# Performance work log

Measured on AMD Instinct MI355X. Metric: run time of the kernel, lower is better.

## Reference

```python
import jax, jax.numpy as jnp
import numpy as np

N = 8192
IN_F = 512
OUT_F = 256
ALPHA = 0.2          # LeakyReLU negative slope
MASK_VAL = -9e15     # same sentinel as the torch code


def setup_inputs() -> dict:
    key = jax.random.key(0)
    k1, k2, k3, k4, k5, k6 = jax.random.split(key, 6)
    inputs = jax.random.normal(k1, (N, IN_F), dtype=jnp.float32)
    # sparse-ish 0/1 dense adjacency (~avg degree 64)
    adj = (jax.random.uniform(k2, (N, N)) < (64.0 / N)).astype(jnp.float32)
    W = jax.random.normal(k3, (IN_F, OUT_F), dtype=jnp.float32) * (1.414 / np.sqrt(IN_F))
    a = jax.random.normal(k4, (2 * OUT_F, 1), dtype=jnp.float32) * 0.1
    W_gc = jax.random.normal(k5, (IN_F, OUT_F), dtype=jnp.float32) * (1.414 / np.sqrt(IN_F))
    b_gc = jax.random.normal(k6, (OUT_F,), dtype=jnp.float32) * 0.01
    return {"inputs": inputs, "adj": adj, "W": W, "a": a, "W_gc": W_gc, "b_gc": b_gc}


def reference(inputs, adj, W, a, W_gc, b_gc):
    # h: [n, F]
    h = inputs @ W
    F = h.shape[1]
    # Fused additive attention: e[i,j] = leaky_relu(a1.h_i + a2.h_j)
    # (mathematically identical to the repeat/cat construction in the source)
    f_src = h @ a[:F, 0]   # [n]
    f_dst = h @ a[F:, 0]   # [n]
    e = jax.nn.leaky_relu(f_src[:, None] + f_dst[None, :], negative_slope=ALPHA)  # [n, n]
    # masked row-softmax over neighbors
    att = jnp.where(adj > 0, e, MASK_VAL)
    att = jax.nn.softmax(att, axis=1)
    # dropout p=0.0 -> identity
    h_prime = att @ h  # [n, F]
    # optional dense graph-convolution branch (graph_convolve=True)
    gc = adj @ (inputs @ W_gc) + b_gc
    return h_prime + gc
```

## Files before the change

kernel.cpp:

```cpp
#include <hip/hip_runtime.h>
#include <hip/hip_bf16.h>
#include <math.h>

#define N_NODES 8192
#define IN_F    512
#define OUT_F   256
#define NCAT    512
#define ALPHA   0.2f
#define MAXDEG  512

typedef __attribute__((ext_vector_type(8))) short short8;
typedef __attribute__((ext_vector_type(4))) float f32x4;

static __device__ __forceinline__ short f2bf(float f) {
    union { float f; unsigned u; } v; v.f = f;
    unsigned r = v.u + 0x7fffu + ((v.u >> 16) & 1u);
    return (short)(r >> 16);
}
static __device__ __forceinline__ float bf2f(short s) {
    union { unsigned u; float f; } v;
    v.u = ((unsigned)(unsigned short)s) << 16;
    return v.f;
}

__global__ __launch_bounds__(512) void bt_pack(const float* __restrict__ W,
                                               const float* __restrict__ W_gc,
                                               short* __restrict__ Bt) {
    const int n = blockIdx.x;
    const int k = threadIdx.x;
    const int c = n >> 1;
    float v = (n & 1) ? W_gc[(size_t)k * OUT_F + c] : W[(size_t)k * OUT_F + c];
    Bt[(size_t)n * IN_F + k] = f2bf(v);
}

__global__ __launch_bounds__(256) void gemm_mfma(const float* __restrict__ A,
                                                 const short* __restrict__ Bt,
                                                 short* __restrict__ hcat) {
    __shared__ short As[128 * 32];
    __shared__ short Bs[128 * 32];

    const int tid  = threadIdx.x;
    const int m0   = blockIdx.y * 128;
    const int n0   = blockIdx.x * 128;
    const int wid  = tid >> 6;
    const int lane = tid & 63;
    const int wr   = wid >> 1;
    const int wc   = wid & 1;
    const int mh   = lane & 15;
    const int q    = lane >> 4;

    const int srow  = tid >> 1;
    const int shalf = tid & 1;

    const f32x4 vzero = {0.f, 0.f, 0.f, 0.f};
    f32x4 acc[4][4];
    #pragma unroll
    for (int i = 0; i < 4; i++)
        #pragma unroll
        for (int j = 0; j < 4; j++) acc[i][j] = vzero;

    const float* aga = A  + (size_t)(m0 + srow) * IN_F + shalf * 16;
    const short* bgb = Bt + (size_t)(n0 + srow) * IN_F + shalf * 16;
    short* asw = &As[srow * 32 + shalf * 16];
    short* bsw = &Bs[srow * 32 + shalf * 16];

    for (int k0 = 0; k0 < IN_F; k0 += 32) {
        const float4* a4 = (const float4*)(aga + k0);
        float4 x0 = a4[0], x1 = a4[1], x2 = a4[2], x3 = a4[3];
        const int4* b4 = (const int4*)(bgb + k0);
        int4 bv0 = b4[0], bv1 = b4[1];

        short8 p0, p1;
        p0[0] = f2bf(x0.x); p0[1] = f2bf(x0.y); p0[2] = f2bf(x0.z); p0[3] = f2bf(x0.w);
        p0[4] = f2bf(x1.x); p0[5] = f2bf(x1.y); p0[6] = f2bf(x1.z); p0[7] = f2bf(x1.w);
        p1[0] = f2bf(x2.x); p1[1] = f2bf(x2.y); p1[2] = f2bf(x2.z); p1[3] = f2bf(x2.w);
        p1[4] = f2bf(x3.x); p1[5] = f2bf(x3.y); p1[6] = f2bf(x3.z); p1[7] = f2bf(x3.w);

        __syncthreads();
        *(short8*)asw       = p0;
        *(short8*)(asw + 8) = p1;
        *(int4*)bsw         = bv0;
        *(int4*)(bsw + 8)   = bv1;
        __syncthreads();

        short8 af[4], bfm[4];
        #pragma unroll
        for (int i = 0; i < 4; i++) {
            af[i]  = *(const short8*)&As[(wr * 64 + i * 16 + mh) * 32 + q * 8];
            bfm[i] = *(const short8*)&Bs[(wc * 64 + i * 16 + mh) * 32 + q * 8];
        }
        #pragma unroll
        for (int mi = 0; mi < 4; mi++)
            #pragma unroll
            for (int ni = 0; ni < 4; ni++)
                acc[mi][ni] = __builtin_amdgcn_mfma_f32_16x16x32_bf16(
                    af[mi], bfm[ni], acc[mi][ni], 0, 0, 0);
    }

    #pragma unroll
    for (int mi = 0; mi < 4; mi++)
        #pragma unroll
        for (int ni = 0; ni < 4; ni++) {
            const int col   = n0 + wc * 64 + ni * 16 + mh;
            const int rbase = m0 + wr * 64 + mi * 16 + q * 4;
            f32x4 v = acc[mi][ni];
            #pragma unroll
            for (int r = 0; r < 4; r++)
                hcat[(size_t)(rbase + r) * NCAT + col] = f2bf(v[r]);
        }
}

__global__ __launch_bounds__(256) void compute_f(const short* __restrict__ hcat,
                                                 const float* __restrict__ a,
                                                 float* __restrict__ f_src,
                                                 float* __restrict__ f_dst) {
    const int row  = blockIdx.x * 4 + (threadIdx.x >> 6);
    const int lane = threadIdx.x & 63;
    const short* hr = hcat + (size_t)row * NCAT;
    float s1 = 0.f, s2 = 0.f;
    #pragma unroll
    for (int c = lane; c < OUT_F; c += 64) {
        float hv = bf2f(hr[2 * c]);
        s1 += hv * a[c];
        s2 += hv * a[OUT_F + c];
    }
    #pragma unroll
    for (int off = 32; off; off >>= 1) {
        s1 += __shfl_down(s1, off);
        s2 += __shfl_down(s2, off);
    }
    if (lane == 0) { f_src[row] = s1; f_dst[row] = s2; }
}

__global__ __launch_bounds__(256) void attn_row(const float* __restrict__ adj,
                                                const short* __restrict__ hcat,
                                                const float* __restrict__ f_src,
                                                const float* __restrict__ f_dst,
                                                const float* __restrict__ b_gc,
                                                float* __restrict__ out) {
    __shared__ int   s_idx[MAXDEG];
    __shared__ float s_w[MAXDEG];
    __shared__ float s_red[8];
    __shared__ int   s_count;

    const int row  = blockIdx.x;
    const int tid  = threadIdx.x;
    const int lane = tid & 63;
    const int wid  = tid >> 6;

    if (tid == 0) s_count = 0;
    __syncthreads();

    const float fs = f_src[row];

    const f32x4* arow4 = (const f32x4*)(adj + (size_t)row * N_NODES);
    float lmax = -INFINITY;
    #pragma unroll
    for (int it = 0; it < N_NODES / 4 / 256; it++) {
        const int c = it * 256 + tid;
        f32x4 v = __builtin_nontemporal_load(arow4 + c);
        int cnt = (v[0] > 0.f) + (v[1] > 0.f) + (v[2] > 0.f) + (v[3] > 0.f);
        if (cnt) {
            int pos = atomicAdd(&s_count, cnt);
            const int j0 = c * 4;
            #pragma unroll
            for (int i = 0; i < 4; i++) {
                if (v[i] > 0.f) {
                    float e = fs + f_dst[j0 + i];
                    e = (e > 0.f) ? e : ALPHA * e;
                    s_idx[pos] = j0 + i;
                    s_w[pos]   = e;
                    pos++;
                    lmax = fmaxf(lmax, e);
                }
            }
        }
    }
    #pragma unroll
    for (int off = 32; off; off >>= 1) lmax = fmaxf(lmax, __shfl_down(lmax, off));
    if (lane == 0) s_red[wid] = lmax;
    __syncthreads();
    const float m   = fmaxf(fmaxf(s_red[0], s_red[1]), fmaxf(s_red[2], s_red[3]));
    const int   deg = min(s_count, MAXDEG);

    float lsum = 0.f;
    for (int k = tid; k < deg; k += 256) {
        float w = __expf(s_w[k] - m);
        s_w[k] = w;
        lsum += w;
    }
    #pragma unroll
    for (int off = 32; off; off >>= 1) lsum += __shfl_down(lsum, off);
    if (lane == 0) s_red[4 + wid] = lsum;
    __syncthreads();
    const float l = s_red[4] + s_red[5] + s_red[6] + s_red[7];
    const float inv_l = (deg > 0) ? 1.f / l : 0.f;

    const int u = lane >> 4;
    const int p = lane & 15;
    const short* hbase = hcat + wid * 128 + p * 8;

    float aa0 = 0.f, aa1 = 0.f, aa2 = 0.f, aa3 = 0.f;
    float gg0 = 0.f, gg1 = 0.f, gg2 = 0.f, gg3 = 0.f;
    #pragma unroll 4
    for (int k = u; k < deg; k += 4) {
        const int   j = s_idx[k];
        const float w = s_w[k];
        short8 v = *(const short8*)(hbase + (size_t)j * NCAT);
        aa0 += w * bf2f(v[0]); gg0 += bf2f(v[1]);
        aa1 += w * bf2f(v[2]); gg1 += bf2f(v[3]);
        aa2 += w * bf2f(v[4]); gg2 += bf2f(v[5]);
        aa3 += w * bf2f(v[6]); gg3 += bf2f(v[7]);
    }
    aa0 += __shfl_down(aa0, 32); aa1 += __shfl_down(aa1, 32);
    aa2 += __shfl_down(aa2, 32); aa3 += __shfl_down(aa3, 32);
    gg0 += __shfl_down(gg0, 32); gg1 += __shfl_down(gg1, 32);
    gg2 += __shfl_down(gg2, 32); gg3 += __shfl_down(gg3, 32);
    aa0 += __shfl_down(aa0, 16); aa1 += __shfl_down(aa1, 16);
    aa2 += __shfl_down(aa2, 16); aa3 += __shfl_down(aa3, 16);
    gg0 += __shfl_down(gg0, 16); gg1 += __shfl_down(gg1, 16);
    gg2 += __shfl_down(gg2, 16); gg3 += __shfl_down(gg3, 16);

    if (u == 0) {
        const int col = wid * 64 + p * 4;
        const float4 bg = *(const float4*)(b_gc + col);
        float4 o;
        o.x = aa0 * inv_l + gg0 + bg.x;
        o.y = aa1 * inv_l + gg1 + bg.y;
        o.z = aa2 * inv_l + gg2 + bg.z;
        o.w = aa3 * inv_l + gg3 + bg.w;
        *(float4*)(out + (size_t)row * OUT_F + col) = o;
    }
}

extern "C" void kernel_launch(void* const* d_in, const int* in_sizes, int n_in,
                              void* d_out, int out_size, void* d_ws, size_t ws_size,
                              hipStream_t stream) {
    const float* inputs = (const float*)d_in[0];
    const float* adj    = (const float*)d_in[1];
    const float* W      = (const float*)d_in[2];
    const float* a      = (const float*)d_in[3];
    const float* W_gc   = (const float*)d_in[4];
    const float* b_gc   = (const float*)d_in[5];
    float* out = (float*)d_out;

    short* Bt    = (short*)d_ws;
    short* hcat  = Bt + (size_t)NCAT * IN_F;
    float* f_src = (float*)(hcat + (size_t)N_NODES * NCAT);
    float* f_dst = f_src + N_NODES;

    bt_pack<<<dim3(NCAT), dim3(IN_F), 0, stream>>>(W, W_gc, Bt);
    gemm_mfma<<<dim3(NCAT / 128, N_NODES / 128), 256, 0, stream>>>(inputs, Bt, hcat);
    compute_f<<<N_NODES / 4, 256, 0, stream>>>(hcat, a, f_src, f_dst);
    attn_row<<<N_NODES, 256, 0, stream>>>(adj, hcat, f_src, f_dst, b_gc, out);
}
```

Measured before the change: 432.5 us.

## Split attention into scan and gather kernels with separate h/g tables

Stores the attention features and graph-conv features in two separate bf16 tables instead of one interleaved buffer. The per-row attention kernel is split into a scan pass, which compacts neighbors and exponentiates scores into a global list, and a gather pass, which aggregates h and g rows separately. The softmax max-subtraction is dropped, which saves a reduction and a barrier but risks overflow for large logits. The split adds a kernel launch and a global round-trip for the neighbor list in exchange for lighter, higher-occupancy kernels.

```diff
diff --git a/kernel.cpp b/kernel.cpp
--- a/kernel.cpp
+++ b/kernel.cpp
@@ -10,6 +10,7 @@
 #define MAXDEG  512
 
 typedef __attribute__((ext_vector_type(8))) short short8;
+typedef __attribute__((ext_vector_type(4))) short short4e;
 typedef __attribute__((ext_vector_type(4))) float f32x4;
 
 static __device__ __forceinline__ short f2bf(float f) {
@@ -28,14 +29,15 @@
                                                short* __restrict__ Bt) {
     const int n = blockIdx.x;
     const int k = threadIdx.x;
-    const int c = n >> 1;
-    float v = (n & 1) ? W_gc[(size_t)k * OUT_F + c] : W[(size_t)k * OUT_F + c];
+    float v = (n < OUT_F) ? W[(size_t)k * OUT_F + n]
+                          : W_gc[(size_t)k * OUT_F + (n - OUT_F)];
     Bt[(size_t)n * IN_F + k] = f2bf(v);
 }
 
 __global__ __launch_bounds__(256) void gemm_mfma(const float* __restrict__ A,
                                                  const short* __restrict__ Bt,
-                                                 short* __restrict__ hcat) {
+                                                 short* __restrict__ h_t,
+                                                 short* __restrict__ g_t) {
     __shared__ short As[128 * 32];
     __shared__ short Bs[128 * 32];
 
@@ -97,32 +99,35 @@
                     af[mi], bfm[ni], acc[mi][ni], 0, 0, 0);
     }
 
+    short* tab  = (n0 < OUT_F) ? h_t : g_t;
+    const int cb = (n0 < OUT_F) ? n0 : n0 - OUT_F;
     #pragma unroll
     for (int mi = 0; mi < 4; mi++)
         #pragma unroll
         for (int ni = 0; ni < 4; ni++) {
-            const int col   = n0 + wc * 64 + ni * 16 + mh;
+            const int col   = cb + wc * 64 + ni * 16 + mh;
             const int rbase = m0 + wr * 64 + mi * 16 + q * 4;
             f32x4 v = acc[mi][ni];
             #pragma unroll
             for (int r = 0; r < 4; r++)
-                hcat[(size_t)(rbase + r) * NCAT + col] = f2bf(v[r]);
+                tab[(size_t)(rbase + r) * OUT_F + col] = f2bf(v[r]);
         }
 }
 
-__global__ __launch_bounds__(256) void compute_f(const short* __restrict__ hcat,
+__global__ __launch_bounds__(256) void compute_f(const short* __restrict__ h_t,
                                                  const float* __restrict__ a,
                                                  float* __restrict__ f_src,
                                                  float* __restrict__ f_dst) {
     const int row  = blockIdx.x * 4 + (threadIdx.x >> 6);
     const int lane = threadIdx.x & 63;
-    const short* hr = hcat + (size_t)row * NCAT;
+    const int c0   = lane * 4;
+    short4e v = *(const short4e*)(h_t + (size_t)row * OUT_F + c0);
     float s1 = 0.f, s2 = 0.f;
     #pragma unroll
-    for (int c = lane; c < OUT_F; c += 64) {
-        float hv = bf2f(hr[2 * c]);
-        s1 += hv * a[c];
-        s2 += hv * a[OUT_F + c];
+    for (int i = 0; i < 4; i++) {
+        float hv = bf2f(v[i]);
+        s1 += hv * a[c0 + i];
+        s2 += hv * a[OUT_F + c0 + i];
     }
     #pragma unroll
     for (int off = 32; off; off >>= 1) {
@@ -132,15 +137,15 @@
     if (lane == 0) { f_src[row] = s1; f_dst[row] = s2; }
 }
 
-__global__ __launch_bounds__(256) void attn_row(const float* __restrict__ adj,
-                                                const short* __restrict__ hcat,
-                                                const float* __restrict__ f_src,
-                                                const float* __restrict__ f_dst,
-                                                const float* __restrict__ b_gc,
-                                                float* __restrict__ out) {
+__global__ __launch_bounds__(256) void attn_scan(const float* __restrict__ adj,
+                                                 const float* __restrict__ f_src,
+                                                 const float* __restrict__ f_dst,
+                                                 int2* __restrict__ list,
+                                                 int* __restrict__ cnt,
+                                                 float* __restrict__ lsum) {
     __shared__ int   s_idx[MAXDEG];
     __shared__ float s_w[MAXDEG];
-    __shared__ float s_red[8];
+    __shared__ float s_red[4];
     __shared__ int   s_count;
 
     const int row  = blockIdx.x;
@@ -152,85 +157,122 @@
     __syncthreads();
 
     const float fs = f_src[row];
-
     const f32x4* arow4 = (const f32x4*)(adj + (size_t)row * N_NODES);
-    float lmax = -INFINITY;
+
+    float lloc = 0.f;
     #pragma unroll
     for (int it = 0; it < N_NODES / 4 / 256; it++) {
         const int c = it * 256 + tid;
         f32x4 v = __builtin_nontemporal_load(arow4 + c);
-        int cnt = (v[0] > 0.f) + (v[1] > 0.f) + (v[2] > 0.f) + (v[3] > 0.f);
-        if (cnt) {
-            int pos = atomicAdd(&s_count, cnt);
+        int c4 = (v[0] > 0.f) + (v[1] > 0.f) + (v[2] > 0.f) + (v[3] > 0.f);
+        if (c4) {
+            int pos = atomicAdd(&s_count, c4);
             const int j0 = c * 4;
             #pragma unroll
             for (int i = 0; i < 4; i++) {
                 if (v[i] > 0.f) {
                     float e = fs + f_dst[j0 + i];
                     e = (e > 0.f) ? e : ALPHA * e;
+                    float w = __expf(e);
                     s_idx[pos] = j0 + i;
-                    s_w[pos]   = e;
+                    s_w[pos]   = w;
                     pos++;
-                    lmax = fmaxf(lmax, e);
+                    lloc += w;
                 }
             }
         }
     }
     #pragma unroll
-    for (int off = 32; off; off >>= 1) lmax = fmaxf(lmax, __shfl_down(lmax, off));
-    if (lane == 0) s_red[wid] = lmax;
-    __syncthreads();
-    const float m   = fmaxf(fmaxf(s_red[0], s_red[1]), fmaxf(s_red[2], s_red[3]));
-    const int   deg = min(s_count, MAXDEG);
-
-    float lsum = 0.f;
+    for (int off = 32; off; off >>= 1) lloc += __shfl_down(lloc, off);
+    if (lane == 0) s_red[wid] = lloc;
+    __syncthreads();
+
+    const int deg = min(s_count, MAXDEG);
+    int2* lrow = list + (size_t)row * MAXDEG;
     for (int k = tid; k < deg; k += 256) {
-        float w = __expf(s_w[k] - m);
-        s_w[k] = w;
-        lsum += w;
-    }
-    #pragma unroll
-    for (int off = 32; off; off >>= 1) lsum += __shfl_down(lsum, off);
-    if (lane == 0) s_red[4 + wid] = lsum;
-    __syncthreads();
-    const float l = s_red[4] + s_red[5] + s_red[6] + s_red[7];
+        int2 e; e.x = s_idx[k]; e.y = __float_as_int(s_w[k]);
+        lrow[k] = e;
+    }
+    if (tid == 0) {
+        cnt[row]  = deg;
+        lsum[row] = s_red[0] + s_red[1] + s_red[2] + s_red[3];
+    }
+}
+
+__global__ __launch_bounds__(256) void attn_gather(const short* __restrict__ h_t,
+                                                   const short* __restrict__ g_t,
+                                                   const int2* __restrict__ list,
+                                                   const int* __restrict__ cnt,
+                                                   const float* __restrict__ lsum,
+                                                   const float* __restrict__ b_gc,
+                                                   float* __restrict__ out) {
+    __shared__ int   s_idx[MAXDEG];
+    __shared__ float s_w[MAXDEG];
+    __shared__ float s_part[4][32][9];
+
+    const int row  = blockIdx.x;
+    const int tid  = threadIdx.x;
+    const int lane = tid & 63;
+    const int wid  = tid >> 6;
+
+    const int   deg   = cnt[row];
+    const float l     = lsum[row];
     const float inv_l = (deg > 0) ? 1.f / l : 0.f;
 
-    const int u = lane >> 4;
-    const int p = lane & 15;
-    const short* hbase = hcat + wid * 128 + p * 8;
-
-    float aa0 = 0.f, aa1 = 0.f, aa2 = 0.f, aa3 = 0.f;
-    float gg0 = 0.f, gg1 = 0.f, gg2 = 0.f, gg3 = 0.f;
+    const int2* lrow = list + (size_t)row * MAXDEG;
+    for (int k = tid; k < deg; k += 256) {
+        int2 e = lrow[k];
+        s_idx[k] = e.x;
+        s_w[k]   = __int_as_float(e.y);
+    }
+    __syncthreads();
+
+    const int sub = lane >> 5;
+    const int p   = lane & 31;
+    const int nb0 = wid * 2 + sub;
+    const short* hb = h_t + p * 8;
+    const short* gb = g_t + p * 8;
+
+    float acc[8] = {0.f, 0.f, 0.f, 0.f, 0.f, 0.f, 0.f, 0.f};
     #pragma unroll 4
-    for (int k = u; k < deg; k += 4) {
+    for (int k = nb0; k < deg; k += 8) {
         const int   j = s_idx[k];
         const float w = s_w[k];
-        short8 v = *(const short8*)(hbase + (size_t)j * NCAT);
-        aa0 += w * bf2f(v[0]); gg0 += bf2f(v[1]);
-        aa1 += w * bf2f(v[2]); gg1 += bf2f(v[3]);
-        aa2 += w * bf2f(v[4]); gg2 += bf2f(v[5]);
-        aa3 += w * bf2f(v[6]); gg3 += bf2f(v[7]);
-    }
-    aa0 += __shfl_down(aa0, 32); aa1 += __shfl_down(aa1, 32);
-    aa2 += __shfl_down(aa2, 32); aa3 += __shfl_down(aa3, 32);
-    gg0 += __shfl_down(gg0, 32); gg1 += __shfl_down(gg1, 32);
-    gg2 += __shfl_down(gg2, 32); gg3 += __shfl_down(gg3, 32);
-    aa0 += __shfl_down(aa0, 16); aa1 += __shfl_down(aa1, 16);
-    aa2 += __shfl_down(aa2, 16); aa3 += __shfl_down(aa3, 16);
-    gg0 += __shfl_down(gg0, 16); gg1 += __shfl_down(gg1, 16);
-    gg2 += __shfl_down(gg2, 16); gg3 += __shfl_down(gg3, 16);
-
-    if (u == 0) {
-        const int col = wid * 64 + p * 4;
-        const float4 bg = *(const float4*)(b_gc + col);
-        float4 o;
-        o.x = aa0 * inv_l + gg0 + bg.x;
-        o.y = aa1 * inv_l + gg1 + bg.y;
-        o.z = aa2 * inv_l + gg2 + bg.z;
-        o.w = aa3 * inv_l + gg3 + bg.w;
-        *(float4*)(out + (size_t)row * OUT_F + col) = o;
-    }
+        short8 v = *(const short8*)(hb + (size_t)j * OUT_F);
+        #pragma unroll
+        for (int i = 0; i < 8; i++) acc[i] += w * bf2f(v[i]);
+    }
+    #pragma unroll
+    for (int i = 0; i < 8; i++) acc[i] += __shfl_down(acc[i], 32);
+    if (sub == 0) {
+        #pragma unroll
+        for (int i = 0; i < 8; i++) s_part[wid][p][i] = acc[i];
+    }
+    __syncthreads();
+    const int pc = tid >> 3, ic = tid & 7;
+    const float hsumv = s_part[0][pc][ic] + s_part[1][pc][ic]
+                      + s_part[2][pc][ic] + s_part[3][pc][ic];
+    __syncthreads();
+
+    float accg[8] = {0.f, 0.f, 0.f, 0.f, 0.f, 0.f, 0.f, 0.f};
+    #pragma unroll 4
+    for (int k = nb0; k < deg; k += 8) {
+        const int j = s_idx[k];
+        short8 v = *(const short8*)(gb + (size_t)j * OUT_F);
+        #pragma unroll
+        for (int i = 0; i < 8; i++) accg[i] += bf2f(v[i]);
+    }
+    #pragma unroll
+    for (int i = 0; i < 8; i++) accg[i] += __shfl_down(accg[i], 32);
+    if (sub == 0) {
+        #pragma unroll
+        for (int i = 0; i < 8; i++) s_part[wid][p][i] = accg[i];
+    }
+    __syncthreads();
+    const float gsumv = s_part[0][pc][ic] + s_part[1][pc][ic]
+                      + s_part[2][pc][ic] + s_part[3][pc][ic];
+
+    out[(size_t)row * OUT_F + tid] = hsumv * inv_l + gsumv + b_gc[tid];
 }
 
 extern "C" void kernel_launch(void* const* d_in, const int* in_sizes, int n_in,
@@ -245,12 +287,17 @@
     float* out = (float*)d_out;
 
     short* Bt    = (short*)d_ws;
-    short* hcat  = Bt + (size_t)NCAT * IN_F;
-    float* f_src = (float*)(hcat + (size_t)N_NODES * NCAT);
+    short* h_t   = Bt + (size_t)NCAT * IN_F;
+    short* g_t   = h_t + (size_t)N_NODES * OUT_F;
+    float* f_src = (float*)(g_t + (size_t)N_NODES * OUT_F);
     float* f_dst = f_src + N_NODES;
+    float* lsum  = f_dst + N_NODES;
+    int*   cnt   = (int*)(lsum + N_NODES);
+    int2*  list  = (int2*)(cnt + N_NODES);
 
     bt_pack<<<dim3(NCAT), dim3(IN_F), 0, stream>>>(W, W_gc, Bt);
-    gemm_mfma<<<dim3(NCAT / 128, N_NODES / 128), 256, 0, stream>>>(inputs, Bt, hcat);
-    compute_f<<<N_NODES / 4, 256, 0, stream>>>(hcat, a, f_src, f_dst);
-    attn_row<<<N_NODES, 256, 0, stream>>>(adj, hcat, f_src, f_dst, b_gc, out);
-}
+    gemm_mfma<<<dim3(NCAT / 128, N_NODES / 128), 256, 0, stream>>>(inputs, Bt, h_t, g_t);
+    compute_f<<<N_NODES / 4, 256, 0, stream>>>(h_t, a, f_src, f_dst);
+    attn_scan<<<N_NODES, 256, 0, stream>>>(adj, f_src, f_dst, list, cnt, lsum);
+    attn_gather<<<N_NODES, 256, 0, stream>>>(h_t, g_t, list, cnt, lsum, b_gc, out);
+}
```

New measurement: 446.9 us. 3.3% more time.
